# Kernel optimization log

Hardware: AMD Instinct MI355X
Metric: run time of the kernel (lower is better)

The kernel has to match this reference:

```python
import jax, jax.numpy as jnp
import numpy as np

B, T, N, V, D = 2048, 50, 100, 50000, 512  # batch, targets/ex, noises/ex (=2*T), vocab, label_size


def setup_inputs() -> dict:
    key = jax.random.key(0)
    k1, k2, k3, k4 = jax.random.split(key, 4)
    features = jax.random.normal(k1, (B, D), dtype=jnp.float32)
    targets = jax.random.randint(k2, (B, T), 0, V, dtype=jnp.int64)
    noises = jax.random.randint(k3, (B, N), 0, V, dtype=jnp.int64)
    W = jax.random.normal(k4, (V, D), dtype=jnp.float32) * 0.02  # h2o.weight [V, D]
    return {"features": features, "targets": targets, "noises": noises, "W": W}


def reference(features, targets, noises, W):
    # Per example: out = concat([W[targets] @ f, -(W[noises] @ f)]);
    # loss_i = -mean(logsigmoid(out)); total = sum_i loss_i. (dropout=0 / eval)
    pos = jnp.einsum('btd,bd->bt', W[targets], features)   # [B, T]
    neg = jnp.einsum('bnd,bd->bn', W[noises], features)    # [B, N]
    ls = jax.nn.log_sigmoid
    per_ex = -(jnp.sum(ls(pos), axis=1) + jnp.sum(ls(-neg), axis=1)) / (T + N)
    return jnp.sum(per_ex)
```

## Files before the change

### kernel.cpp

```cpp
#include <hip/hip_runtime.h>
#include <math.h>

constexpr int B_   = 2048;
constexpr int T_   = 50;
constexpr int N_   = 100;
constexpr int V_   = 50000;
constexpr int D_   = 512;
constexpr int NTOT = T_ + N_;
constexpr int CAP  = 48;


__global__ __launch_bounds__(256) void scatter_kernel(
    const int* __restrict__ targets,
    const int* __restrict__ noises,
    unsigned int* __restrict__ counts,
    unsigned int* __restrict__ bucket)
{
    const int gid = blockIdx.x * 256 + threadIdx.x;
    int v; unsigned int e;
    if (gid < B_ * T_) {
        v = targets[gid];
        e = (unsigned int)(gid / T_) << 1;
    } else if (gid < B_ * T_ + B_ * N_) {
        const int g2 = gid - B_ * T_;
        v = noises[g2];
        e = ((unsigned int)(g2 / N_) << 1) | 1u;
    } else {
        return;
    }
    const unsigned int pos = atomicAdd(&counts[v], 1u);
    if (pos < CAP) bucket[(size_t)v * CAP + pos] = e;
}

__global__ __launch_bounds__(256) void nsl_main(
    const float* __restrict__ features,
    const float* __restrict__ W,
    const unsigned int* __restrict__ counts,
    const unsigned int* __restrict__ bucket,
    float* __restrict__ out)
{
    const int tid  = threadIdx.x;
    const int lane = tid & 63;
    const int wave = tid >> 6;
    const int wgid = blockIdx.x * 4 + wave;
    const int nw   = gridDim.x * 4;

    float acc = 0.f;

    for (int v = wgid; v < V_; v += nw) {
        const int cnt = min((int)counts[v], CAP);
        if (cnt == 0) continue;

        const float4* w4 = reinterpret_cast<const float4*>(W + (size_t)v * D_);
        const float4 wa = w4[lane];
        const float4 wb = w4[lane + 64];
        const unsigned int* bk = bucket + (size_t)v * CAP;

        for (int c = 0; c < cnt; c += 8) {
            float p[8];
            unsigned int smask = 0;
            #pragma unroll
            for (int j = 0; j < 8; ++j) {
                if (c + j < cnt) {
                    const unsigned int e = bk[c + j];
                    smask |= (e & 1u) << j;
                    const float4* f4 = reinterpret_cast<const float4*>(
                        features + (size_t)(e >> 1) * D_);
                    const float4 fa = f4[lane];
                    const float4 fb = f4[lane + 64];
                    p[j] = wa.x * fa.x + wa.y * fa.y + wa.z * fa.z + wa.w * fa.w
                         + wb.x * fb.x + wb.y * fb.y + wb.z * fb.z + wb.w * fb.w;
                } else {
                    p[j] = 0.f;
                }
            }

            #pragma unroll
            for (int j = 0; j < 4; ++j) {
                const float a = p[2 * j], cc = p[2 * j + 1];
                const float own = (lane & 1) ? cc : a;
                const float oth = (lane & 1) ? a : cc;
                p[j] = own + __shfl_xor(oth, 1, 64);
            }
            #pragma unroll
            for (int j = 0; j < 2; ++j) {
                const float a = p[2 * j], cc = p[2 * j + 1];
                const float own = (lane & 2) ? cc : a;
                const float oth = (lane & 2) ? a : cc;
                p[j] = own + __shfl_xor(oth, 2, 64);
            }
            {
                const float a = p[0], cc = p[1];
                const float own = (lane & 4) ? cc : a;
                const float oth = (lane & 4) ? a : cc;
                p[0] = own + __shfl_xor(oth, 4, 64);
            }
            float q = p[0];
            q += __shfl_xor(q, 8, 64);
            q += __shfl_xor(q, 16, 64);
            q += __shfl_xor(q, 32, 64);

            const int rl = lane & 7;
            const float x  = ((smask >> rl) & 1u) ? -q : q;
            const float ls = fminf(x, 0.f) - __logf(1.f + __expf(-fabsf(x)));
            if (c + rl < cnt) acc += ls;
        }
    }

    #pragma unroll
    for (int s = 32; s >= 1; s >>= 1)
        acc += __shfl_xor(acc, s, 64);

    __shared__ float s_wsum[4];
    if (lane == 0) s_wsum[wave] = acc;
    __syncthreads();
    if (tid == 0) {
        const float s = s_wsum[0] + s_wsum[1] + s_wsum[2] + s_wsum[3];
        atomicAdd(out, -s / (8.0f * (float)NTOT));
    }
}

constexpr int NPAD = 152;
constexpr int NCHK = NPAD / 8;

__global__ __launch_bounds__(256, 8) void nsl_fallback(
    const float* __restrict__ features,
    const int* __restrict__ targets,
    const int* __restrict__ noises,
    const float* __restrict__ W,
    float* __restrict__ out)
{
    const int b    = blockIdx.x;
    const int tid  = threadIdx.x;
    const int lane = tid & 63;
    const int wave = tid >> 6;

    __shared__ int   s_idx[NPAD];
    __shared__ float s_wsum[4];

    if (tid < T_)          s_idx[tid] = targets[(size_t)b * T_ + tid];
    else if (tid < NTOT)   s_idx[tid] = noises[(size_t)b * N_ + (tid - T_)];
    else if (tid < NPAD)   s_idx[tid] = 0;
    __syncthreads();

    const float4* f4 = reinterpret_cast<const float4*>(features + (size_t)b * D_);
    const float4 fa = f4[lane];
    const float4 fb = f4[lane + 64];

    float acc = 0.f;
    for (int k = wave; k < NCHK; k += 4) {
        float p[8];
        #pragma unroll
        for (int j = 0; j < 8; ++j) {
            const int idx = s_idx[8 * k + j];
            const float4* w4 = reinterpret_cast<const float4*>(W + (size_t)idx * D_);
            const float4 wa = w4[lane];
            const float4 wb = w4[lane + 64];
            p[j] = wa.x * fa.x + wa.y * fa.y + wa.z * fa.z + wa.w * fa.w
                 + wb.x * fb.x + wb.y * fb.y + wb.z * fb.z + wb.w * fb.w;
        }
        #pragma unroll
        for (int j = 0; j < 4; ++j) {
            const float a = p[2 * j], c = p[2 * j + 1];
            const float own = (lane & 1) ? c : a;
            const float oth = (lane & 1) ? a : c;
            p[j] = own + __shfl_xor(oth, 1, 64);
        }
        #pragma unroll
        for (int j = 0; j < 2; ++j) {
            const float a = p[2 * j], c = p[2 * j + 1];
            const float own = (lane & 2) ? c : a;
            const float oth = (lane & 2) ? a : c;
            p[j] = own + __shfl_xor(oth, 2, 64);
        }
        {
            const float a = p[0], c = p[1];
            const float own = (lane & 4) ? c : a;
            const float oth = (lane & 4) ? a : c;
            p[0] = own + __shfl_xor(oth, 4, 64);
        }
        float q = p[0];
        q += __shfl_xor(q, 8, 64);
        q += __shfl_xor(q, 16, 64);
        q += __shfl_xor(q, 32, 64);

        const int r = 8 * k + (lane & 7);
        const float x  = (r < T_) ? q : -q;
        const float ls = fminf(x, 0.f) - __logf(1.f + __expf(-fabsf(x)));
        if (r < NTOT) acc += ls;
    }

    #pragma unroll
    for (int s = 32; s >= 1; s >>= 1)
        acc += __shfl_xor(acc, s, 64);

    if (lane == 0) s_wsum[wave] = acc;
    __syncthreads();
    if (tid == 0) {
        const float s = s_wsum[0] + s_wsum[1] + s_wsum[2] + s_wsum[3];
        atomicAdd(out, -s / (8.0f * (float)NTOT));
    }
}

extern "C" void kernel_launch(void* const* d_in, const int* in_sizes, int n_in,
                              void* d_out, int out_size, void* d_ws, size_t ws_size,
                              hipStream_t stream) {
    const float* features = (const float*)d_in[0];
    const int*   targets  = (const int*)d_in[1];
    const int*   noises   = (const int*)d_in[2];
    const float* W        = (const float*)d_in[3];
    float*       out      = (float*)d_out;

    hipMemsetAsync(out, 0, sizeof(float), stream);

    const size_t counts_bytes = (size_t)V_ * sizeof(unsigned int);
    const size_t bucket_bytes = (size_t)V_ * CAP * sizeof(unsigned int);
    const size_t need = counts_bytes + bucket_bytes;

    if (ws_size >= need) {
        unsigned int* counts = (unsigned int*)d_ws;
        unsigned int* bucket = (unsigned int*)((char*)d_ws + counts_bytes);

        hipMemsetAsync(counts, 0, counts_bytes, stream);

        const int total = B_ * T_ + B_ * N_;
        scatter_kernel<<<(total + 255) / 256, 256, 0, stream>>>(
            targets, noises, counts, bucket);

        nsl_main<<<2048, 256, 0, stream>>>(features, W, counts, bucket, out);
    } else {
        nsl_fallback<<<B_, 256, 0, stream>>>(features, targets, noises, W, out);
    }
}
```

Before: 229.9 us.

## Batch feature loads, fix grid to vocab size, replace atomics with partial reduction

The main kernel now issues all eight bucket-entry reads and all eight feature-row loads before doing the dot products, so more memory requests are in flight per wave. The grid is set so each wave handles exactly four vocab rows, using a fixed stride instead of a grid-stride loop, and occupancy is hinted via launch bounds. The final atomic accumulation into the output is replaced by per-block partial sums plus a single-block reduce kernel, which removes the output memset. This costs more registers per thread and one extra kernel launch.

After: 221.5 us. 3.6% less time.

```diff
diff --git a/kernel.cpp b/kernel.cpp
--- a/kernel.cpp
+++ b/kernel.cpp
@@ -8,6 +8,8 @@
 constexpr int D_   = 512;
 constexpr int NTOT = T_ + N_;
 constexpr int CAP  = 48;
+
+constexpr int GRID_MAIN = 3125;
 
 
 __global__ __launch_bounds__(256) void scatter_kernel(
@@ -32,22 +34,23 @@
     if (pos < CAP) bucket[(size_t)v * CAP + pos] = e;
 }
 
-__global__ __launch_bounds__(256) void nsl_main(
+__global__ __launch_bounds__(256, 4) void nsl_main(
     const float* __restrict__ features,
     const float* __restrict__ W,
     const unsigned int* __restrict__ counts,
     const unsigned int* __restrict__ bucket,
-    float* __restrict__ out)
+    float* __restrict__ partial)
 {
     const int tid  = threadIdx.x;
     const int lane = tid & 63;
     const int wave = tid >> 6;
     const int wgid = blockIdx.x * 4 + wave;
-    const int nw   = gridDim.x * 4;
 
     float acc = 0.f;
 
-    for (int v = wgid; v < V_; v += nw) {
+    #pragma unroll
+    for (int rr = 0; rr < 4; ++rr) {
+        const int v = wgid + rr * 12500;
         const int cnt = min((int)counts[v], CAP);
         if (cnt == 0) continue;
 
@@ -57,22 +60,29 @@
         const unsigned int* bk = bucket + (size_t)v * CAP;
 
         for (int c = 0; c < cnt; c += 8) {
+            unsigned int e[8];
+            #pragma unroll
+            for (int j = 0; j < 8; ++j)
+                e[j] = bk[(c + j < cnt) ? (c + j) : c];
+
+            unsigned int smask = 0;
+            #pragma unroll
+            for (int j = 0; j < 8; ++j) smask |= (e[j] & 1u) << j;
+
+            float4 fa[8], fb[8];
+            #pragma unroll
+            for (int j = 0; j < 8; ++j) {
+                const float4* f4 = reinterpret_cast<const float4*>(
+                    features + (size_t)(e[j] >> 1) * D_);
+                fa[j] = f4[lane];
+                fb[j] = f4[lane + 64];
+            }
+
             float p[8];
-            unsigned int smask = 0;
             #pragma unroll
             for (int j = 0; j < 8; ++j) {
-                if (c + j < cnt) {
-                    const unsigned int e = bk[c + j];
-                    smask |= (e & 1u) << j;
-                    const float4* f4 = reinterpret_cast<const float4*>(
-                        features + (size_t)(e >> 1) * D_);
-                    const float4 fa = f4[lane];
-                    const float4 fb = f4[lane + 64];
-                    p[j] = wa.x * fa.x + wa.y * fa.y + wa.z * fa.z + wa.w * fa.w
-                         + wb.x * fb.x + wb.y * fb.y + wb.z * fb.z + wb.w * fb.w;
-                } else {
-                    p[j] = 0.f;
-                }
+                p[j] = wa.x * fa[j].x + wa.y * fa[j].y + wa.z * fa[j].z + wa.w * fa[j].w
+                     + wb.x * fb[j].x + wb.y * fb[j].y + wb.z * fb[j].z + wb.w * fb[j].w;
             }
 
             #pragma unroll
@@ -114,9 +124,27 @@
     __shared__ float s_wsum[4];
     if (lane == 0) s_wsum[wave] = acc;
     __syncthreads();
+    if (tid == 0)
+        partial[blockIdx.x] = s_wsum[0] + s_wsum[1] + s_wsum[2] + s_wsum[3];
+}
+
+__global__ __launch_bounds__(256) void reduce_kernel(
+    const float* __restrict__ partial, float* __restrict__ out)
+{
+    const int tid  = threadIdx.x;
+    const int lane = tid & 63;
+    const int wave = tid >> 6;
+    float s = 0.f;
+    for (int i = tid; i < GRID_MAIN; i += 256) s += partial[i];
+    #pragma unroll
+    for (int sh = 32; sh >= 1; sh >>= 1)
+        s += __shfl_xor(s, sh, 64);
+    __shared__ float s_wsum[4];
+    if (lane == 0) s_wsum[wave] = s;
+    __syncthreads();
     if (tid == 0) {
-        const float s = s_wsum[0] + s_wsum[1] + s_wsum[2] + s_wsum[3];
-        atomicAdd(out, -s / (8.0f * (float)NTOT));
+        const float tot = s_wsum[0] + s_wsum[1] + s_wsum[2] + s_wsum[3];
+        out[0] = -tot / (8.0f * (float)NTOT);
     }
 }
 
@@ -211,15 +239,15 @@
     const float* W        = (const float*)d_in[3];
     float*       out      = (float*)d_out;
 
-    hipMemsetAsync(out, 0, sizeof(float), stream);
-
-    const size_t counts_bytes = (size_t)V_ * sizeof(unsigned int);
-    const size_t bucket_bytes = (size_t)V_ * CAP * sizeof(unsigned int);
-    const size_t need = counts_bytes + bucket_bytes;
+    const size_t counts_bytes  = (size_t)V_ * sizeof(unsigned int);
+    const size_t bucket_bytes  = (size_t)V_ * CAP * sizeof(unsigned int);
+    const size_t partial_bytes = (size_t)GRID_MAIN * sizeof(float);
+    const size_t need = counts_bytes + bucket_bytes + partial_bytes;
 
     if (ws_size >= need) {
-        unsigned int* counts = (unsigned int*)d_ws;
-        unsigned int* bucket = (unsigned int*)((char*)d_ws + counts_bytes);
+        unsigned int* counts  = (unsigned int*)d_ws;
+        unsigned int* bucket  = (unsigned int*)((char*)d_ws + counts_bytes);
+        float*        partial = (float*)((char*)d_ws + counts_bytes + bucket_bytes);
 
         hipMemsetAsync(counts, 0, counts_bytes, stream);
 
@@ -227,8 +255,10 @@
         scatter_kernel<<<(total + 255) / 256, 256, 0, stream>>>(
             targets, noises, counts, bucket);
 
-        nsl_main<<<2048, 256, 0, stream>>>(features, W, counts, bucket, out);
+        nsl_main<<<GRID_MAIN, 256, 0, stream>>>(features, W, counts, bucket, partial);
+        reduce_kernel<<<1, 256, 0, stream>>>(partial, out);
     } else {
+        hipMemsetAsync(out, 0, sizeof(float), stream);
         nsl_fallback<<<B_, 256, 0, stream>>>(features, targets, noises, W, out);
     }
 }
```
